# Kernel tuning notes

Hardware: AMD Instinct MI355X
Metric: run time of the kernel (lower is better)

The kernel has to match this reference:

```python
import jax, jax.numpy as jnp
import numpy as np

INPUT_SIZE = 24
HIDDEN = 128
N_LAYERS = 2
OUT_SIZE = 1


def setup_inputs() -> dict:
    key = jax.random.key(0)
    ks = jax.random.split(key, 2 + 4 * N_LAYERS + 2)
    x = jax.random.normal(ks[0], (2048, 128, INPUT_SIZE), dtype=jnp.float32)
    params = {}
    s = 1.0 / np.sqrt(HIDDEN)
    idx = 1
    for l in range(N_LAYERS):
        in_dim = INPUT_SIZE if l == 0 else HIDDEN
        params[f"W_ih{l}"] = jax.random.uniform(ks[idx], (4 * HIDDEN, in_dim), minval=-s, maxval=s, dtype=jnp.float32); idx += 1
        params[f"W_hh{l}"] = jax.random.uniform(ks[idx], (4 * HIDDEN, HIDDEN), minval=-s, maxval=s, dtype=jnp.float32); idx += 1
        params[f"b_ih{l}"] = jax.random.uniform(ks[idx], (4 * HIDDEN,), minval=-s, maxval=s, dtype=jnp.float32); idx += 1
        params[f"b_hh{l}"] = jax.random.uniform(ks[idx], (4 * HIDDEN,), minval=-s, maxval=s, dtype=jnp.float32); idx += 1
    params["W_fc"] = jax.random.uniform(ks[idx], (OUT_SIZE, HIDDEN), minval=-s, maxval=s, dtype=jnp.float32); idx += 1
    params["b_fc"] = jax.random.uniform(ks[idx], (OUT_SIZE,), minval=-s, maxval=s, dtype=jnp.float32)
    return {"x": x, **params}


def _lstm_layer(x, W_ih, W_hh, b_ih, b_hh):
    # x: [B, T, in] -> outputs [B, T, H]. PyTorch gate order: i, f, g, o.
    B = x.shape[0]
    H = W_hh.shape[1]
    # precompute input projections for all timesteps: [T, B, 4H]
    xproj = jnp.einsum('bti,gi->tbg', x, W_ih) + b_ih + b_hh

    def step(carry, xp_t):
        h, c = carry
        gates = xp_t + h @ W_hh.T  # [B, 4H]
        i, f, g, o = jnp.split(gates, 4, axis=-1)
        i = jax.nn.sigmoid(i)
        f = jax.nn.sigmoid(f)
        g = jnp.tanh(g)
        o = jax.nn.sigmoid(o)
        c = f * c + i * g
        h = o * jnp.tanh(c)
        return (h, c), h

    h0 = jnp.zeros((B, H), dtype=x.dtype)
    c0 = jnp.zeros((B, H), dtype=x.dtype)
    (_, _), hs = jax.lax.scan(step, (h0, c0), xproj)
    return jnp.transpose(hs, (1, 0, 2))  # [B, T, H]


def reference(x, W_ih0, W_hh0, b_ih0, b_hh0, W_ih1, W_hh1, b_ih1, b_hh1, W_fc, b_fc):
    # Inference-mode forward: inter-layer dropout (p=0.2) is identity in eval.
    h1 = _lstm_layer(x, W_ih0, W_hh0, b_ih0, b_hh0)   # [B, T, H]
    h2 = _lstm_layer(h1, W_ih1, W_hh1, b_ih1, b_hh1)  # [B, T, H]
    last = h2[:, -1, :]                               # [B, H]
    return last @ W_fc.T + b_fc                       # [B, 1]
```

## Files before the change

kernel.cpp:

```cpp
#include <hip/hip_runtime.h>

#define TSTEPS 128
#define NIN 24
#define HD 128
#define BT 16
#define NBLK 128
#define NTH 512

#define RS    136
#define SLOT  (BT*RS)
#define XS    40
#define XTS   (BT*XS)
#define XBUF  (8*XTS)
#define RINGN 9

#define RING_OFF 0
#define XB_OFF   (RINGN*SLOT)
#define SM_SIZE  (XB_OFF + 2*XBUF)

#define HB_OFF 0
#define B2_OFF (8*SLOT)

typedef _Float16 half8  __attribute__((ext_vector_type(8)));
typedef _Float16 half4v __attribute__((ext_vector_type(4)));
typedef float    floatx4 __attribute__((ext_vector_type(4)));

__device__ __forceinline__ float sigf(float x) {
    return __builtin_amdgcn_rcpf(1.0f + __expf(-x));
}
__device__ __forceinline__ float tanh_f(float x) {
    return 1.0f - 2.0f * __builtin_amdgcn_rcpf(1.0f + __expf(2.0f * x));
}

__device__ __forceinline__ half8 ldw8(const float* p) {
    const float4* q = (const float4*)p;
    float4 a = q[0], b = q[1];
    half8 r;
    r[0] = (_Float16)a.x; r[1] = (_Float16)a.y; r[2] = (_Float16)a.z; r[3] = (_Float16)a.w;
    r[4] = (_Float16)b.x; r[5] = (_Float16)b.y; r[6] = (_Float16)b.z; r[7] = (_Float16)b.w;
    return r;
}

__global__ __launch_bounds__(NTH, 2)
void lstm2_fused(const float* __restrict__ x,
                 const float* __restrict__ Wih0, const float* __restrict__ Whh0,
                 const float* __restrict__ bih0, const float* __restrict__ bhh0,
                 const float* __restrict__ Wih1, const float* __restrict__ Whh1,
                 const float* __restrict__ bih1, const float* __restrict__ bhh1,
                 const float* __restrict__ Wfc,  const float* __restrict__ bfc,
                 float* __restrict__ out, _Float16* __restrict__ h1ws)
{
    __shared__ __align__(16) _Float16 SM[SM_SIZE];

    const int tid = threadIdx.x;
    const int blk = blockIdx.x;
    const int wv  = tid >> 6;
    const int ln  = tid & 63;
    const int qd  = ln >> 4;
    const int nn  = ln & 15;
    const int b0  = blk * BT;
    const size_t wsbase = (size_t)blk * (TSTEPS * BT * HD);

    const half8 z8 = {0, 0, 0, 0, 0, 0, 0, 0};

    for (int i = tid * 8; i < SM_SIZE; i += NTH * 8) *(half8*)&SM[i] = z8;

    float bias0[4], bias1[4];
#pragma unroll
    for (int tI = 0; tI < 4; ++tI) {
        int g = tI * HD + wv * 16 + nn;
        bias0[tI] = bih0[g] + bhh0[g];
        bias1[tI] = bih1[g] + bhh1[g];
    }

    half8 wih0[4];
    half8 whh0[4][4];
#pragma unroll
    for (int tI = 0; tI < 4; ++tI) {
        int g = tI * HD + wv * 16 + nn;
        if (qd < 3) wih0[tI] = ldw8(Wih0 + g * NIN + qd * 8);
        else        wih0[tI] = z8;
#pragma unroll
        for (int kk = 0; kk < 4; ++kk)
            whh0[tI][kk] = ldw8(Whh0 + g * HD + kk * 32 + qd * 8);
    }

    __syncthreads();

    {
        const int c = 0, buf = 0;
        for (int i = tid; i < 8 * BT * 6; i += NTH) {
            int ti = i / 96, r = i % 96, b = r / 6, q = r % 6;
            float4 v = *(const float4*)(x + (size_t)(b0 + b) * (TSTEPS * NIN)
                                          + (size_t)(c * 8 + ti) * NIN + q * 4);
            half4v h; h[0] = (_Float16)v.x; h[1] = (_Float16)v.y;
                      h[2] = (_Float16)v.z; h[3] = (_Float16)v.w;
            *(half4v*)&SM[XB_OFF + buf * XBUF + ti * XTS + b * XS + q * 4] = h;
        }
    }

    float cs0[4] = {0.f, 0.f, 0.f, 0.f};
    const int jc = wv * 16 + nn;

#pragma unroll 1
    for (int t = 0; t < TSTEPS; ++t) {
        __syncthreads();

        if ((t & 7) == 0) {
            if (t + 8 < TSTEPS) {
                const int c = (t >> 3) + 1, buf = c & 1;
                for (int i = tid; i < 8 * BT * 6; i += NTH) {
                    int ti = i / 96, r = i % 96, b = r / 6, q = r % 6;
                    float4 v = *(const float4*)(x + (size_t)(b0 + b) * (TSTEPS * NIN)
                                                  + (size_t)(c * 8 + ti) * NIN + q * 4);
                    half4v h; h[0] = (_Float16)v.x; h[1] = (_Float16)v.y;
                              h[2] = (_Float16)v.z; h[3] = (_Float16)v.w;
                    *(half4v*)&SM[XB_OFF + buf * XBUF + ti * XTS + b * XS + q * 4] = h;
                }
            }
            if (t > 0) {
                const int c = (t >> 3) - 1;
#pragma unroll
                for (int k = 0; k < 4; ++k) {
                    int e  = tid + k * NTH;
                    int ti = e >> 8;
                    int r  = e & 255;
                    int b  = r >> 4;
                    int c8 = (r & 15) * 8;
                    int tau = c * 8 + ti;
                    half8 v = *(const half8*)&SM[RING_OFF + (tau % 9) * SLOT + b * RS + c8];
                    *(half8*)(h1ws + wsbase + ((size_t)tau * BT + b) * HD + c8) = v;
                }
            }
        }

        const half8 ax = *(const half8*)&SM[XB_OFF + ((t >> 3) & 1) * XBUF
                                            + (t & 7) * XTS + nn * XS + qd * 8];
        const int sprev = (t + 8) % 9;
        half8 ah[4];
#pragma unroll
        for (int kk = 0; kk < 4; ++kk)
            ah[kk] = *(const half8*)&SM[RING_OFF + sprev * SLOT + nn * RS + kk * 32 + qd * 8];

        floatx4 acc[4];
#pragma unroll
        for (int tI = 0; tI < 4; ++tI) {
            floatx4 a = {bias0[tI], bias0[tI], bias0[tI], bias0[tI]};
            a = __builtin_amdgcn_mfma_f32_16x16x32_f16(ax, wih0[tI], a, 0, 0, 0);
#pragma unroll
            for (int kk = 0; kk < 4; ++kk)
                a = __builtin_amdgcn_mfma_f32_16x16x32_f16(ah[kk], whh0[tI][kk], a, 0, 0, 0);
            acc[tI] = a;
        }

        const int scur = t % 9;
#pragma unroll
        for (int r = 0; r < 4; ++r) {
            float iv = sigf(acc[0][r]);
            float fv = sigf(acc[1][r]);
            float gv = tanh_f(acc[2][r]);
            float ov = sigf(acc[3][r]);
            float cn = fv * cs0[r] + iv * gv;
            cs0[r] = cn;
            float hv = ov * tanh_f(cn);
            SM[RING_OFF + scur * SLOT + (qd * 4 + r) * RS + jc] = (_Float16)hv;
        }
    }

    __syncthreads();
    {
        const int c = 15;
#pragma unroll
        for (int k = 0; k < 4; ++k) {
            int e  = tid + k * NTH;
            int ti = e >> 8;
            int r  = e & 255;
            int b  = r >> 4;
            int c8 = (r & 15) * 8;
            int tau = c * 8 + ti;
            half8 v = *(const half8*)&SM[RING_OFF + (tau % 9) * SLOT + b * RS + c8];
            *(half8*)(h1ws + wsbase + ((size_t)tau * BT + b) * HD + c8) = v;
        }
    }

    half8 wih1[4][4], whh1[4][4];
#pragma unroll
    for (int tI = 0; tI < 4; ++tI) {
        int g = tI * HD + wv * 16 + nn;
#pragma unroll
        for (int kk = 0; kk < 4; ++kk) {
            wih1[tI][kk] = ldw8(Wih1 + g * HD + kk * 32 + qd * 8);
            whh1[tI][kk] = ldw8(Whh1 + g * HD + kk * 32 + qd * 8);
        }
    }

    __syncthreads();

    for (int i = tid * 8; i < 2 * SLOT; i += NTH * 8) *(half8*)&SM[B2_OFF + i] = z8;
    {
        const int c = 0, buf = 0;
#pragma unroll
        for (int k = 0; k < 2; ++k) {
            int e  = tid + k * NTH;
            int ti = e >> 8;
            int r  = e & 255;
            int b  = r >> 4;
            int c8 = (r & 15) * 8;
            half8 v = *(const half8*)(h1ws + wsbase + ((size_t)(c * 4 + ti) * BT + b) * HD + c8);
            *(half8*)&SM[HB_OFF + buf * (4 * SLOT) + ti * SLOT + b * RS + c8] = v;
        }
    }

    float cs1[4] = {0.f, 0.f, 0.f, 0.f};

#pragma unroll 1
    for (int tau = 0; tau < TSTEPS; ++tau) {
        __syncthreads();

        if ((tau & 3) == 0 && tau + 4 < TSTEPS) {
            const int c = (tau >> 2) + 1, buf = c & 1;
#pragma unroll
            for (int k = 0; k < 2; ++k) {
                int e  = tid + k * NTH;
                int ti = e >> 8;
                int r  = e & 255;
                int b  = r >> 4;
                int c8 = (r & 15) * 8;
                half8 v = *(const half8*)(h1ws + wsbase + ((size_t)(c * 4 + ti) * BT + b) * HD + c8);
                *(half8*)&SM[HB_OFF + buf * (4 * SLOT) + ti * SLOT + b * RS + c8] = v;
            }
        }

        const int cur = tau & 1, nxt = cur ^ 1;
        const int hbase = HB_OFF + ((tau >> 2) & 1) * (4 * SLOT) + (tau & 3) * SLOT;

        half8 a1[4], a2[4];
#pragma unroll
        for (int kk = 0; kk < 4; ++kk) {
            a1[kk] = *(const half8*)&SM[hbase + nn * RS + kk * 32 + qd * 8];
            a2[kk] = *(const half8*)&SM[B2_OFF + cur * SLOT + nn * RS + kk * 32 + qd * 8];
        }

        floatx4 acc[4];
#pragma unroll
        for (int tI = 0; tI < 4; ++tI) {
            floatx4 a = {bias1[tI], bias1[tI], bias1[tI], bias1[tI]};
#pragma unroll
            for (int kk = 0; kk < 4; ++kk)
                a = __builtin_amdgcn_mfma_f32_16x16x32_f16(a1[kk], wih1[tI][kk], a, 0, 0, 0);
#pragma unroll
            for (int kk = 0; kk < 4; ++kk)
                a = __builtin_amdgcn_mfma_f32_16x16x32_f16(a2[kk], whh1[tI][kk], a, 0, 0, 0);
            acc[tI] = a;
        }

#pragma unroll
        for (int r = 0; r < 4; ++r) {
            float iv = sigf(acc[0][r]);
            float fv = sigf(acc[1][r]);
            float gv = tanh_f(acc[2][r]);
            float ov = sigf(acc[3][r]);
            float cn = fv * cs1[r] + iv * gv;
            cs1[r] = cn;
            float hv = ov * tanh_f(cn);
            SM[B2_OFF + nxt * SLOT + (qd * 4 + r) * RS + jc] = (_Float16)hv;
        }
    }
    __syncthreads();

    {
        int b = tid >> 5, sub = tid & 31;
        const _Float16* hp = &SM[B2_OFF + b * RS + sub * 4];
        const float4 wv4 = *(const float4*)(Wfc + sub * 4);
        float s = (float)hp[0] * wv4.x + (float)hp[1] * wv4.y
                + (float)hp[2] * wv4.z + (float)hp[3] * wv4.w;
        s += __shfl_down(s, 16, 32);
        s += __shfl_down(s, 8, 32);
        s += __shfl_down(s, 4, 32);
        s += __shfl_down(s, 2, 32);
        s += __shfl_down(s, 1, 32);
        if (sub == 0) out[b0 + b] = s + bfc[0];
    }
}

extern "C" void kernel_launch(void* const* d_in, const int* in_sizes, int n_in,
                              void* d_out, int out_size, void* d_ws, size_t ws_size,
                              hipStream_t stream) {
    const float* x    = (const float*)d_in[0];
    const float* Wih0 = (const float*)d_in[1];
    const float* Whh0 = (const float*)d_in[2];
    const float* bih0 = (const float*)d_in[3];
    const float* bhh0 = (const float*)d_in[4];
    const float* Wih1 = (const float*)d_in[5];
    const float* Whh1 = (const float*)d_in[6];
    const float* bih1 = (const float*)d_in[7];
    const float* bhh1 = (const float*)d_in[8];
    const float* Wfc  = (const float*)d_in[9];
    const float* bfc  = (const float*)d_in[10];
    float* out = (float*)d_out;
    _Float16* h1ws = (_Float16*)d_ws;

    lstm2_fused<<<dim3(NBLK), dim3(NTH), 0, stream>>>(
        x, Wih0, Whh0, bih0, bhh0, Wih1, Whh1, bih1, bhh1, Wfc, bfc, out, h1ws);
}
```

Measured before the change: 372.2 us.

## Wavefront-fuse both LSTM layers into one time loop, staging Whh1 in LDS

Layer 1 now runs one step behind layer 0 inside a single time loop, so the two recurrences interleave and only one barrier per step covers both. This removes the global h1 workspace round trip and the second serial 128-step loop. Whh1 is moved from registers into a swizzled LDS layout read every step, to keep register pressure manageable now that three weight sets would otherwise be live. x is prefetched per step straight into registers instead of being staged in LDS. The cost is extra LDS reads per step and a large dynamic shared memory allocation (about 140KB), which may cut occupancy.

```diff
diff --git a/kernel.cpp b/kernel.cpp
--- a/kernel.cpp
+++ b/kernel.cpp
@@ -9,17 +9,10 @@
 
 #define RS    136
 #define SLOT  (BT*RS)
-#define XS    40
-#define XTS   (BT*XS)
-#define XBUF  (8*XTS)
-#define RINGN 9
-
-#define RING_OFF 0
-#define XB_OFF   (RINGN*SLOT)
-#define SM_SIZE  (XB_OFF + 2*XBUF)
-
-#define HB_OFF 0
-#define B2_OFF (8*SLOT)
+#define H1B   (2*SLOT)
+#define W1B   (4*SLOT)
+#define SM_ELTS (W1B + 8*16*512)
+#define SM_BYTES (SM_ELTS*2)
 
 typedef _Float16 half8  __attribute__((ext_vector_type(8)));
 typedef _Float16 half4v __attribute__((ext_vector_type(4)));
@@ -48,9 +41,9 @@
                  const float* __restrict__ Wih1, const float* __restrict__ Whh1,
                  const float* __restrict__ bih1, const float* __restrict__ bhh1,
                  const float* __restrict__ Wfc,  const float* __restrict__ bfc,
-                 float* __restrict__ out, _Float16* __restrict__ h1ws)
+                 float* __restrict__ out)
 {
-    __shared__ __align__(16) _Float16 SM[SM_SIZE];
+    extern __shared__ __align__(16) _Float16 SM[];
 
     const int tid = threadIdx.x;
     const int blk = blockIdx.x;
@@ -59,218 +52,183 @@
     const int qd  = ln >> 4;
     const int nn  = ln & 15;
     const int b0  = blk * BT;
-    const size_t wsbase = (size_t)blk * (TSTEPS * BT * HD);
+    const int jc  = wv * 16 + nn;
 
     const half8 z8 = {0, 0, 0, 0, 0, 0, 0, 0};
 
-    for (int i = tid * 8; i < SM_SIZE; i += NTH * 8) *(half8*)&SM[i] = z8;
+    for (int i = tid * 8; i < W1B; i += NTH * 8) *(half8*)&SM[i] = z8;
 
     float bias0[4], bias1[4];
+    half8 wih0[4];
+    half8 whh0[4][4];
+    half8 wih1[4][4];
 #pragma unroll
     for (int tI = 0; tI < 4; ++tI) {
         int g = tI * HD + wv * 16 + nn;
         bias0[tI] = bih0[g] + bhh0[g];
         bias1[tI] = bih1[g] + bhh1[g];
-    }
-
-    half8 wih0[4];
-    half8 whh0[4][4];
-#pragma unroll
-    for (int tI = 0; tI < 4; ++tI) {
-        int g = tI * HD + wv * 16 + nn;
-        if (qd < 3) wih0[tI] = ldw8(Wih0 + g * NIN + qd * 8);
-        else        wih0[tI] = z8;
-#pragma unroll
-        for (int kk = 0; kk < 4; ++kk)
+        wih0[tI] = (qd < 3) ? ldw8(Wih0 + g * NIN + qd * 8) : z8;
+#pragma unroll
+        for (int kk = 0; kk < 4; ++kk) {
             whh0[tI][kk] = ldw8(Whh0 + g * HD + kk * 32 + qd * 8);
-    }
+            wih1[tI][kk] = ldw8(Wih1 + g * HD + kk * 32 + qd * 8);
+        }
+    }
+
+    for (int i = tid; i < 512 * 32; i += NTH) {
+        int g  = i >> 5;
+        int k0 = (i & 31) << 2;
+        float4 v = *(const float4*)(Whh1 + g * HD + k0);
+        half4v h; h[0] = (_Float16)v.x; h[1] = (_Float16)v.y;
+                  h[2] = (_Float16)v.z; h[3] = (_Float16)v.w;
+        int dst = W1B + ((((g >> 4) & 7) * 16) + (g >> 7) * 4 + (k0 >> 5)) * 512
+                      + (((k0 >> 3) & 3) * 16 + (g & 15)) * 8 + (k0 & 7);
+        *(half4v*)&SM[dst] = h;
+    }
+
+    const float* xrow = x + (size_t)(b0 + nn) * (TSTEPS * NIN) + (qd < 3 ? qd * 8 : 16);
+    float4 pf0 = *(const float4*)(xrow);
+    float4 pf1 = *(const float4*)(xrow + 4);
+
+    float cs0[4] = {0.f, 0.f, 0.f, 0.f};
+    float cs1[4] = {0.f, 0.f, 0.f, 0.f};
+    const int w1base = W1B + wv * 8192 + ln * 8;
 
     __syncthreads();
 
     {
-        const int c = 0, buf = 0;
-        for (int i = tid; i < 8 * BT * 6; i += NTH) {
-            int ti = i / 96, r = i % 96, b = r / 6, q = r % 6;
-            float4 v = *(const float4*)(x + (size_t)(b0 + b) * (TSTEPS * NIN)
-                                          + (size_t)(c * 8 + ti) * NIN + q * 4);
-            half4v h; h[0] = (_Float16)v.x; h[1] = (_Float16)v.y;
-                      h[2] = (_Float16)v.z; h[3] = (_Float16)v.w;
-            *(half4v*)&SM[XB_OFF + buf * XBUF + ti * XTS + b * XS + q * 4] = h;
-        }
-    }
-
-    float cs0[4] = {0.f, 0.f, 0.f, 0.f};
-    const int jc = wv * 16 + nn;
+        half8 ax;
+        ax[0] = (_Float16)pf0.x; ax[1] = (_Float16)pf0.y; ax[2] = (_Float16)pf0.z; ax[3] = (_Float16)pf0.w;
+        ax[4] = (_Float16)pf1.x; ax[5] = (_Float16)pf1.y; ax[6] = (_Float16)pf1.z; ax[7] = (_Float16)pf1.w;
+        pf0 = *(const float4*)(xrow + NIN);
+        pf1 = *(const float4*)(xrow + NIN + 4);
+
+        floatx4 acc0[4];
+#pragma unroll
+        for (int tI = 0; tI < 4; ++tI) {
+            floatx4 a0 = {bias0[tI], bias0[tI], bias0[tI], bias0[tI]};
+            acc0[tI] = __builtin_amdgcn_mfma_f32_16x16x32_f16(ax, wih0[tI], a0, 0, 0, 0);
+        }
+#pragma unroll
+        for (int r = 0; r < 4; ++r) {
+            float iv = sigf(acc0[0][r]);
+            float gv = tanh_f(acc0[2][r]);
+            float ov = sigf(acc0[3][r]);
+            float cn = iv * gv;
+            cs0[r] = cn;
+            SM[(qd * 4 + r) * RS + jc] = (_Float16)(ov * tanh_f(cn));
+        }
+    }
 
 #pragma unroll 1
-    for (int t = 0; t < TSTEPS; ++t) {
+    for (int t = 1; t < TSTEPS; ++t) {
         __syncthreads();
 
-        if ((t & 7) == 0) {
-            if (t + 8 < TSTEPS) {
-                const int c = (t >> 3) + 1, buf = c & 1;
-                for (int i = tid; i < 8 * BT * 6; i += NTH) {
-                    int ti = i / 96, r = i % 96, b = r / 6, q = r % 6;
-                    float4 v = *(const float4*)(x + (size_t)(b0 + b) * (TSTEPS * NIN)
-                                                  + (size_t)(c * 8 + ti) * NIN + q * 4);
-                    half4v h; h[0] = (_Float16)v.x; h[1] = (_Float16)v.y;
-                              h[2] = (_Float16)v.z; h[3] = (_Float16)v.w;
-                    *(half4v*)&SM[XB_OFF + buf * XBUF + ti * XTS + b * XS + q * 4] = h;
-                }
+        half8 ax;
+        ax[0] = (_Float16)pf0.x; ax[1] = (_Float16)pf0.y; ax[2] = (_Float16)pf0.z; ax[3] = (_Float16)pf0.w;
+        ax[4] = (_Float16)pf1.x; ax[5] = (_Float16)pf1.y; ax[6] = (_Float16)pf1.z; ax[7] = (_Float16)pf1.w;
+        {
+            const int tn = (t < TSTEPS - 1) ? t + 1 : TSTEPS - 1;
+            pf0 = *(const float4*)(xrow + tn * NIN);
+            pf1 = *(const float4*)(xrow + tn * NIN + 4);
+        }
+
+        const int h0r = ((t - 1) & 1) * SLOT;
+        const int h0w = (t & 1) * SLOT;
+        const int h1r = H1B + (t & 1) * SLOT;
+        const int h1w = H1B + ((t & 1) ^ 1) * SLOT;
+
+        floatx4 acc0[4], acc1[4];
+#pragma unroll
+        for (int tI = 0; tI < 4; ++tI) {
+            floatx4 a0 = {bias0[tI], bias0[tI], bias0[tI], bias0[tI]};
+            acc0[tI] = __builtin_amdgcn_mfma_f32_16x16x32_f16(ax, wih0[tI], a0, 0, 0, 0);
+            floatx4 a1 = {bias1[tI], bias1[tI], bias1[tI], bias1[tI]};
+            acc1[tI] = a1;
+        }
+
+#pragma unroll
+        for (int kk = 0; kk < 4; ++kk) {
+            const half8 ah = *(const half8*)&SM[h0r + nn * RS + kk * 32 + qd * 8];
+#pragma unroll
+            for (int tI = 0; tI < 4; ++tI)
+                acc0[tI] = __builtin_amdgcn_mfma_f32_16x16x32_f16(ah, whh0[tI][kk], acc0[tI], 0, 0, 0);
+#pragma unroll
+            for (int tI = 0; tI < 4; ++tI)
+                acc1[tI] = __builtin_amdgcn_mfma_f32_16x16x32_f16(ah, wih1[tI][kk], acc1[tI], 0, 0, 0);
+        }
+
+#pragma unroll
+        for (int kk = 0; kk < 4; ++kk) {
+            const half8 a2 = *(const half8*)&SM[h1r + nn * RS + kk * 32 + qd * 8];
+#pragma unroll
+            for (int tI = 0; tI < 4; ++tI) {
+                const half8 w1 = *(const half8*)&SM[w1base + (tI * 4 + kk) * 512];
+                acc1[tI] = __builtin_amdgcn_mfma_f32_16x16x32_f16(a2, w1, acc1[tI], 0, 0, 0);
             }
-            if (t > 0) {
-                const int c = (t >> 3) - 1;
-#pragma unroll
-                for (int k = 0; k < 4; ++k) {
-                    int e  = tid + k * NTH;
-                    int ti = e >> 8;
-                    int r  = e & 255;
-                    int b  = r >> 4;
-                    int c8 = (r & 15) * 8;
-                    int tau = c * 8 + ti;
-                    half8 v = *(const half8*)&SM[RING_OFF + (tau % 9) * SLOT + b * RS + c8];
-                    *(half8*)(h1ws + wsbase + ((size_t)tau * BT + b) * HD + c8) = v;
-                }
-            }
-        }
-
-        const half8 ax = *(const half8*)&SM[XB_OFF + ((t >> 3) & 1) * XBUF
-                                            + (t & 7) * XTS + nn * XS + qd * 8];
-        const int sprev = (t + 8) % 9;
-        half8 ah[4];
-#pragma unroll
-        for (int kk = 0; kk < 4; ++kk)
-            ah[kk] = *(const half8*)&SM[RING_OFF + sprev * SLOT + nn * RS + kk * 32 + qd * 8];
-
-        floatx4 acc[4];
-#pragma unroll
-        for (int tI = 0; tI < 4; ++tI) {
-            floatx4 a = {bias0[tI], bias0[tI], bias0[tI], bias0[tI]};
-            a = __builtin_amdgcn_mfma_f32_16x16x32_f16(ax, wih0[tI], a, 0, 0, 0);
-#pragma unroll
-            for (int kk = 0; kk < 4; ++kk)
-                a = __builtin_amdgcn_mfma_f32_16x16x32_f16(ah[kk], whh0[tI][kk], a, 0, 0, 0);
-            acc[tI] = a;
-        }
-
-        const int scur = t % 9;
-#pragma unroll
-        for (int r = 0; r < 4; ++r) {
-            float iv = sigf(acc[0][r]);
-            float fv = sigf(acc[1][r]);
-            float gv = tanh_f(acc[2][r]);
-            float ov = sigf(acc[3][r]);
+        }
+
+#pragma unroll
+        for (int r = 0; r < 4; ++r) {
+            float iv = sigf(acc0[0][r]);
+            float fv = sigf(acc0[1][r]);
+            float gv = tanh_f(acc0[2][r]);
+            float ov = sigf(acc0[3][r]);
             float cn = fv * cs0[r] + iv * gv;
             cs0[r] = cn;
-            float hv = ov * tanh_f(cn);
-            SM[RING_OFF + scur * SLOT + (qd * 4 + r) * RS + jc] = (_Float16)hv;
-        }
-    }
-
-    __syncthreads();
-    {
-        const int c = 15;
-#pragma unroll
-        for (int k = 0; k < 4; ++k) {
-            int e  = tid + k * NTH;
-            int ti = e >> 8;
-            int r  = e & 255;
-            int b  = r >> 4;
-            int c8 = (r & 15) * 8;
-            int tau = c * 8 + ti;
-            half8 v = *(const half8*)&SM[RING_OFF + (tau % 9) * SLOT + b * RS + c8];
-            *(half8*)(h1ws + wsbase + ((size_t)tau * BT + b) * HD + c8) = v;
-        }
-    }
-
-    half8 wih1[4][4], whh1[4][4];
-#pragma unroll
-    for (int tI = 0; tI < 4; ++tI) {
-        int g = tI * HD + wv * 16 + nn;
-#pragma unroll
-        for (int kk = 0; kk < 4; ++kk) {
-            wih1[tI][kk] = ldw8(Wih1 + g * HD + kk * 32 + qd * 8);
-            whh1[tI][kk] = ldw8(Whh1 + g * HD + kk * 32 + qd * 8);
-        }
-    }
-
-    __syncthreads();
-
-    for (int i = tid * 8; i < 2 * SLOT; i += NTH * 8) *(half8*)&SM[B2_OFF + i] = z8;
-    {
-        const int c = 0, buf = 0;
-#pragma unroll
-        for (int k = 0; k < 2; ++k) {
-            int e  = tid + k * NTH;
-            int ti = e >> 8;
-            int r  = e & 255;
-            int b  = r >> 4;
-            int c8 = (r & 15) * 8;
-            half8 v = *(const half8*)(h1ws + wsbase + ((size_t)(c * 4 + ti) * BT + b) * HD + c8);
-            *(half8*)&SM[HB_OFF + buf * (4 * SLOT) + ti * SLOT + b * RS + c8] = v;
-        }
-    }
-
-    float cs1[4] = {0.f, 0.f, 0.f, 0.f};
-
-#pragma unroll 1
-    for (int tau = 0; tau < TSTEPS; ++tau) {
-        __syncthreads();
-
-        if ((tau & 3) == 0 && tau + 4 < TSTEPS) {
-            const int c = (tau >> 2) + 1, buf = c & 1;
-#pragma unroll
-            for (int k = 0; k < 2; ++k) {
-                int e  = tid + k * NTH;
-                int ti = e >> 8;
-                int r  = e & 255;
-                int b  = r >> 4;
-                int c8 = (r & 15) * 8;
-                half8 v = *(const half8*)(h1ws + wsbase + ((size_t)(c * 4 + ti) * BT + b) * HD + c8);
-                *(half8*)&SM[HB_OFF + buf * (4 * SLOT) + ti * SLOT + b * RS + c8] = v;
-            }
-        }
-
-        const int cur = tau & 1, nxt = cur ^ 1;
-        const int hbase = HB_OFF + ((tau >> 2) & 1) * (4 * SLOT) + (tau & 3) * SLOT;
-
-        half8 a1[4], a2[4];
-#pragma unroll
-        for (int kk = 0; kk < 4; ++kk) {
-            a1[kk] = *(const half8*)&SM[hbase + nn * RS + kk * 32 + qd * 8];
-            a2[kk] = *(const half8*)&SM[B2_OFF + cur * SLOT + nn * RS + kk * 32 + qd * 8];
-        }
-
-        floatx4 acc[4];
-#pragma unroll
-        for (int tI = 0; tI < 4; ++tI) {
-            floatx4 a = {bias1[tI], bias1[tI], bias1[tI], bias1[tI]};
-#pragma unroll
-            for (int kk = 0; kk < 4; ++kk)
-                a = __builtin_amdgcn_mfma_f32_16x16x32_f16(a1[kk], wih1[tI][kk], a, 0, 0, 0);
-#pragma unroll
-            for (int kk = 0; kk < 4; ++kk)
-                a = __builtin_amdgcn_mfma_f32_16x16x32_f16(a2[kk], whh1[tI][kk], a, 0, 0, 0);
-            acc[tI] = a;
-        }
-
-#pragma unroll
-        for (int r = 0; r < 4; ++r) {
-            float iv = sigf(acc[0][r]);
-            float fv = sigf(acc[1][r]);
-            float gv = tanh_f(acc[2][r]);
-            float ov = sigf(acc[3][r]);
+            SM[h0w + (qd * 4 + r) * RS + jc] = (_Float16)(ov * tanh_f(cn));
+        }
+#pragma unroll
+        for (int r = 0; r < 4; ++r) {
+            float iv = sigf(acc1[0][r]);
+            float fv = sigf(acc1[1][r]);
+            float gv = tanh_f(acc1[2][r]);
+            float ov = sigf(acc1[3][r]);
             float cn = fv * cs1[r] + iv * gv;
             cs1[r] = cn;
-            float hv = ov * tanh_f(cn);
-            SM[B2_OFF + nxt * SLOT + (qd * 4 + r) * RS + jc] = (_Float16)hv;
+            SM[h1w + (qd * 4 + r) * RS + jc] = (_Float16)(ov * tanh_f(cn));
+        }
+    }
+
+    {
+        __syncthreads();
+        floatx4 acc1[4];
+#pragma unroll
+        for (int tI = 0; tI < 4; ++tI) {
+            floatx4 a1 = {bias1[tI], bias1[tI], bias1[tI], bias1[tI]};
+            acc1[tI] = a1;
+        }
+#pragma unroll
+        for (int kk = 0; kk < 4; ++kk) {
+            const half8 ah = *(const half8*)&SM[SLOT + nn * RS + kk * 32 + qd * 8];
+#pragma unroll
+            for (int tI = 0; tI < 4; ++tI)
+                acc1[tI] = __builtin_amdgcn_mfma_f32_16x16x32_f16(ah, wih1[tI][kk], acc1[tI], 0, 0, 0);
+        }
+#pragma unroll
+        for (int kk = 0; kk < 4; ++kk) {
+            const half8 a2 = *(const half8*)&SM[H1B + nn * RS + kk * 32 + qd * 8];
+#pragma unroll
+            for (int tI = 0; tI < 4; ++tI) {
+                const half8 w1 = *(const half8*)&SM[w1base + (tI * 4 + kk) * 512];
+                acc1[tI] = __builtin_amdgcn_mfma_f32_16x16x32_f16(a2, w1, acc1[tI], 0, 0, 0);
+            }
+        }
+#pragma unroll
+        for (int r = 0; r < 4; ++r) {
+            float iv = sigf(acc1[0][r]);
+            float fv = sigf(acc1[1][r]);
+            float gv = tanh_f(acc1[2][r]);
+            float ov = sigf(acc1[3][r]);
+            float cn = fv * cs1[r] + iv * gv;
+            SM[H1B + SLOT + (qd * 4 + r) * RS + jc] = (_Float16)(ov * tanh_f(cn));
         }
     }
     __syncthreads();
 
     {
         int b = tid >> 5, sub = tid & 31;
-        const _Float16* hp = &SM[B2_OFF + b * RS + sub * 4];
+        const _Float16* hp = &SM[H1B + SLOT + b * RS + sub * 4];
         const float4 wv4 = *(const float4*)(Wfc + sub * 4);
         float s = (float)hp[0] * wv4.x + (float)hp[1] * wv4.y
                 + (float)hp[2] * wv4.z + (float)hp[3] * wv4.w;
@@ -286,6 +244,12 @@
 extern "C" void kernel_launch(void* const* d_in, const int* in_sizes, int n_in,
                               void* d_out, int out_size, void* d_ws, size_t ws_size,
                               hipStream_t stream) {
+    static bool attr_set = false;
+    if (!attr_set) {
+        hipFuncSetAttribute(reinterpret_cast<const void*>(&lstm2_fused),
+                            hipFuncAttributeMaxDynamicSharedMemorySize, SM_BYTES);
+        attr_set = true;
+    }
     const float* x    = (const float*)d_in[0];
     const float* Wih0 = (const float*)d_in[1];
     const float* Whh0 = (const float*)d_in[2];
@@ -298,8 +262,7 @@
     const float* Wfc  = (const float*)d_in[9];
     const float* bfc  = (const float*)d_in[10];
     float* out = (float*)d_out;
-    _Float16* h1ws = (_Float16*)d_ws;
-
-    lstm2_fused<<<dim3(NBLK), dim3(NTH), 0, stream>>>(
-        x, Wih0, Whh0, bih0, bhh0, Wih1, Whh1, bih1, bhh1, Wfc, bfc, out, h1ws);
-}
+
+    lstm2_fused<<<dim3(NBLK), dim3(NTH), SM_BYTES, stream>>>(
+        x, Wih0, Whh0, bih0, bhh0, Wih1, Whh1, bih1, bhh1, Wfc, bfc, out);
+}
```

New measurement: 365.9 us. About the same (-1.7%).
